# Kernel optimization log

Measured on AMD Instinct MI355X. Metric: run time of the kernel, lower is better.

## Reference

```python
import jax, jax.numpy as jnp
import numpy as np

B, T, D, H = 2, 2048, 1024, 16  # batch, seq, hidden, heads; head_dim = 64


def setup_inputs() -> dict:
    key = jax.random.key(0)
    k1, k2, k3 = jax.random.split(key, 3)
    X = jax.random.normal(k1, (B, T, D), dtype=jnp.float32)
    # Dense(3*hidden_dim, use_bias=False): kernel [D, 3D]
    Wqkv = jax.random.normal(k2, (D, 3 * D), dtype=jnp.float32) / np.float32(np.sqrt(D))
    # Dense(hidden_dim, use_bias=False): kernel [D, D]
    Wproj = jax.random.normal(k3, (D, D), dtype=jnp.float32) / np.float32(np.sqrt(D))
    return {"X": X, "Wqkv": Wqkv, "Wproj": Wproj, "train": 0}


def reference(X, Wqkv, Wproj, train):
    # train=0 -> dropout is identity; the chunked online-softmax in the
    # original is mathematically exact softmax causal attention.
    b, t, d = X.shape
    hd = d // H
    qkv = X @ Wqkv                      # [B,T,3D]
    q, k, v = jnp.split(qkv, 3, axis=-1)
    q = q.reshape(b, t, H, hd)
    k = k.reshape(b, t, H, hd)
    v = v.reshape(b, t, H, hd)
    scale = 1.0 / jnp.sqrt(jnp.asarray(hd, dtype=X.dtype))
    scores = jnp.einsum('bqhd,bkhd->bhqk', q * scale, k)  # [B,H,T,T]
    causal = jnp.tril(jnp.ones((t, t), dtype=bool))
    scores = jnp.where(causal[None, None, :, :], scores, -jnp.inf)
    attn = jax.nn.softmax(scores, axis=-1)
    out = jnp.einsum('bhqk,bkhd->bqhd', attn, v).reshape(b, t, d)
    return out @ Wproj
```

## Files before the change

### kernel.cpp

```cpp
#include <hip/hip_runtime.h>


using u16 = unsigned short;
using u32 = unsigned int;

typedef __bf16 bf16x8 __attribute__((ext_vector_type(8)));
typedef __bf16 bf16x2 __attribute__((ext_vector_type(2)));
typedef float f32x4 __attribute__((ext_vector_type(4)));

#define DEV __device__ __forceinline__

DEV u16 f2bf(float f) { __bf16 h = (__bf16)f; return *(u16*)&h; }

DEV u32 pk2(float lo, float hi) {
  bf16x2 t = {(__bf16)lo, (__bf16)hi};
  return *(u32*)&t;
}

DEV f32x4 mfma16(bf16x8 a, bf16x8 b, f32x4 c) {
  return __builtin_amdgcn_mfma_f32_16x16x32_bf16(a, b, c, 0, 0, 0);
}

DEV void gload_lds16(const void* g, void* l) {
  __builtin_amdgcn_global_load_lds(
      (const __attribute__((address_space(1))) void*)g,
      (__attribute__((address_space(3))) void*)l, 16, 0, 0);
}

DEV bf16x8 ld16(const u16* p) { return *(const bf16x8*)p; }

DEV void BAR() {
  __builtin_amdgcn_s_barrier();
  __builtin_amdgcn_sched_barrier(0);
}

DEV int vperm(int slot) {
  return ((((slot >> 4) & 2) | ((slot >> 2) & 1)) << 4) + (((slot >> 3) & 3) << 2) + (slot & 3);
}


__global__ __launch_bounds__(256) void cvt_x_kernel(const float* __restrict__ X,
                                                    u16* __restrict__ Xb) {
  int i = (blockIdx.x * 256 + threadIdx.x) * 8;
  float4 a = *(const float4*)&X[i];
  float4 b = *(const float4*)&X[i + 4];
  union { u16 u[8]; uint4 v; } o;
  o.u[0] = f2bf(a.x); o.u[1] = f2bf(a.y); o.u[2] = f2bf(a.z); o.u[3] = f2bf(a.w);
  o.u[4] = f2bf(b.x); o.u[5] = f2bf(b.y); o.u[6] = f2bf(b.z); o.u[7] = f2bf(b.w);
  *(uint4*)&Xb[i] = o.v;
}

__global__ __launch_bounds__(256) void transpose_w_kernel(const float* __restrict__ W,
                                                          u16* __restrict__ Wt,
                                                          int R, int C) {
  __shared__ float tile[64][65];
  int tilesC = C >> 6;
  int tr = blockIdx.x / tilesC, tc = blockIdx.x % tilesC;
  int t = threadIdx.x;
#pragma unroll
  for (int j = 0; j < 16; ++j) {
    int idx = j * 256 + t;
    int r = idx >> 6, c = idx & 63;
    tile[r][c] = W[(tr * 64 + r) * C + tc * 64 + c];
  }
  __syncthreads();
#pragma unroll
  for (int j = 0; j < 16; ++j) {
    int idx = j * 256 + t;
    int r = idx >> 6, c = idx & 63;
    Wt[(tc * 64 + r) * R + tr * 64 + c] = f2bf(tile[c][r]);
  }
}

__global__ __launch_bounds__(256) void transpose_v_kernel(const u16* __restrict__ V,
                                                          u16* __restrict__ Vt) {
  __shared__ u16 tile[64 * 65];
  int head = blockIdx.x >> 5, tt = blockIdx.x & 31;
  const u16* src = V + ((size_t)head * 2048 + tt * 64) * 64;
  u16* dst = Vt + (size_t)head * 64 * 2048 + tt * 64;
  int t = threadIdx.x;
#pragma unroll
  for (int it = 0; it < 2; ++it) {
    int idx = it * 2048 + t * 8;
    int r = idx >> 6, c = idx & 63;
    union { uint4 v; u16 u[8]; } tmp;
    tmp.v = *(const uint4*)&src[idx];
#pragma unroll
    for (int j = 0; j < 8; ++j) tile[r * 65 + c + j] = tmp.u[j];
  }
  __syncthreads();
#pragma unroll
  for (int it = 0; it < 2; ++it) {
    int idx = it * 2048 + t * 8;
    int d = idx >> 6, s0 = idx & 63;
    union { uint4 v; u16 u[8]; } tmp;
#pragma unroll
    for (int j = 0; j < 8; ++j) tmp.u[j] = tile[vperm(s0 + j) * 65 + d];
    *(uint4*)&dst[(size_t)d * 2048 + s0] = tmp.v;
  }
}


__global__ __launch_bounds__(512, 2) void gemm256_qkv_kernel(
    const u16* __restrict__ A, const u16* __restrict__ Bt,
    u16* __restrict__ Qb, u16* __restrict__ Kb, u16* __restrict__ Vb) {
  int bid = blockIdx.x;
  int bid2 = (bid & 7) * 24 + (bid >> 3);
  const int mt = bid2 / 12, nt = bid2 % 12;
  const int m0 = mt * 256, n0 = nt * 256;
  const int tid = threadIdx.x;
  const int wid = tid >> 6, lane = tid & 63;
  const int g = lane >> 4, li = lane & 15;
  const int wm = wid >> 2, wn = wid & 3;

  __shared__ __align__(16) u16 lds[65536];

  const int srow = lane >> 3;
  const int scol = ((lane & 7) * 8) ^ ((srow & 7) << 3);

  auto ISSUE = [&](int s, int kt) {
    const int p = kt & 1;
    const u16* base = (s < 2) ? &A[(size_t)(m0 + s * 128) * 1024]
                              : &Bt[(size_t)(n0 + (s - 2) * 128) * 1024];
#pragma unroll
    for (int is2 = 0; is2 < 2; ++is2) {
      int row = is2 * 64 + wid * 8 + srow;
      gload_lds16(&base[(size_t)row * 1024 + kt * 64 + scol],
                  &lds[s * 16384 + p * 8192 + is2 * 4096 + wid * 512]);
    }
  };

  auto LDA = [&](int p, int ks, bf16x8* aF) {
#pragma unroll
    for (int mi = 0; mi < 8; ++mi) {
      int row = mi * 16 + li;
      aF[mi] = ld16(&lds[wm * 16384 + p * 8192 + row * 64 +
                         ((ks * 32 + g * 8) ^ ((li & 7) << 3))]);
    }
  };
  auto LDB = [&](int p, int ks, bf16x8* bF) {
    int s = 2 + (wn >> 1);
#pragma unroll
    for (int ni = 0; ni < 4; ++ni) {
      int row = (wn & 1) * 64 + ni * 16 + li;
      bF[ni] = ld16(&lds[s * 16384 + p * 8192 + row * 64 +
                         ((ks * 32 + g * 8) ^ ((li & 7) << 3))]);
    }
  };

  f32x4 acc[8][4] = {};
  bf16x8 a0[8], a1[8], bF[4];

  ISSUE(0, 0); ISSUE(1, 0); ISSUE(2, 0); ISSUE(3, 0);
  ISSUE(0, 1); ISSUE(1, 1); ISSUE(2, 1);
  asm volatile("s_waitcnt vmcnt(6)" ::: "memory");
  BAR();

  for (int t = 0; t < 16; ++t) {
    const int p = t & 1;
    LDB(p, 0, bF);
    LDA(p, 0, a0);
    if (t + 1 < 16) ISSUE(3, t + 1);
    BAR();
    __builtin_amdgcn_s_setprio(1);
#pragma unroll
    for (int mi = 0; mi < 8; ++mi) {
      acc[mi][0] = mfma16(a0[mi], bF[0], acc[mi][0]);
      acc[mi][1] = mfma16(a0[mi], bF[1], acc[mi][1]);
    }
    __builtin_amdgcn_s_setprio(0);
    BAR();
    LDA(p, 1, a1);
    BAR();
    __builtin_amdgcn_s_setprio(1);
#pragma unroll
    for (int mi = 0; mi < 8; ++mi) {
      acc[mi][2] = mfma16(a0[mi], bF[2], acc[mi][2]);
      acc[mi][3] = mfma16(a0[mi], bF[3], acc[mi][3]);
    }
    __builtin_amdgcn_s_setprio(0);
    BAR();
    LDB(p, 1, bF);
    BAR();
    __builtin_amdgcn_s_setprio(1);
#pragma unroll
    for (int mi = 0; mi < 8; ++mi) {
      acc[mi][0] = mfma16(a1[mi], bF[0], acc[mi][0]);
      acc[mi][1] = mfma16(a1[mi], bF[1], acc[mi][1]);
    }
    __builtin_amdgcn_s_setprio(0);
    BAR();
    if (t + 2 < 16) { ISSUE(0, t + 2); ISSUE(1, t + 2); ISSUE(2, t + 2); }
    BAR();
    __builtin_amdgcn_s_setprio(1);
#pragma unroll
    for (int mi = 0; mi < 8; ++mi) {
      acc[mi][2] = mfma16(a1[mi], bF[2], acc[mi][2]);
      acc[mi][3] = mfma16(a1[mi], bF[3], acc[mi][3]);
    }
    __builtin_amdgcn_s_setprio(0);
    if (t + 2 < 16) {
      asm volatile("s_waitcnt vmcnt(6)" ::: "memory");
    } else {
      asm volatile("s_waitcnt vmcnt(0)" ::: "memory");
    }
    BAR();
  }

#pragma unroll
  for (int mi = 0; mi < 8; ++mi)
#pragma unroll
    for (int ni = 0; ni < 4; ++ni)
#pragma unroll
      for (int r = 0; r < 4; ++r) {
        int rr = m0 + wm * 128 + mi * 16 + g * 4 + r;
        int cc = n0 + wn * 64 + ni * 16 + li;
        float v = acc[mi][ni][r];
        int which = cc >> 10, rem = cc & 1023;
        int h = rem >> 6, dd = rem & 63;
        int bb = rr >> 11, tt = rr & 2047;
        size_t di = ((size_t)(bb * 16 + h) * 2048 + tt) * 64 + dd;
        u16 o = f2bf(which == 0 ? v * 0.18033688f : v);
        (which == 0 ? Qb : which == 1 ? Kb : Vb)[di] = o;
      }
}

__global__ __launch_bounds__(256) void gemm_proj_kernel(
    const u16* __restrict__ A, const u16* __restrict__ Bt, float* __restrict__ OF) {
  constexpr int NTN = 1024 / 128;
  const int mt = blockIdx.x / NTN, nt = blockIdx.x % NTN;
  const int m0 = mt * 128, n0 = nt * 128;
  const int tid = threadIdx.x;
  const int wid = tid >> 6, lane = tid & 63;
  const int g = lane >> 4, li = lane & 15;
  const int wm = wid >> 1, wn = wid & 1;

  __shared__ __align__(16) u16 As[128 * 64];
  __shared__ __align__(16) u16 Bs[128 * 64];

  f32x4 acc[4][4] = {};

  for (int kt = 0; kt < 1024 / 64; ++kt) {
    __syncthreads();
#pragma unroll
    for (int iss = 0; iss < 4; ++iss) {
      int e = iss * 2048 + wid * 512 + lane * 8;
      int row = e >> 6, kk = e & 63;
      gload_lds16(&A[(size_t)(m0 + row) * 1024 + kt * 64 + kk], &As[iss * 2048 + wid * 512]);
      gload_lds16(&Bt[(size_t)(n0 + row) * 1024 + kt * 64 + kk], &Bs[iss * 2048 + wid * 512]);
    }
    __syncthreads();
#pragma unroll
    for (int ks = 0; ks < 2; ++ks) {
      bf16x8 af[4], bfr[4];
#pragma unroll
      for (int mi = 0; mi < 4; ++mi)
        af[mi] = ld16(&As[(wm * 64 + mi * 16 + li) * 64 + ks * 32 + g * 8]);
#pragma unroll
      for (int ni = 0; ni < 4; ++ni)
        bfr[ni] = ld16(&Bs[(wn * 64 + ni * 16 + li) * 64 + ks * 32 + g * 8]);
#pragma unroll
      for (int mi = 0; mi < 4; ++mi)
#pragma unroll
        for (int ni = 0; ni < 4; ++ni)
          acc[mi][ni] = mfma16(af[mi], bfr[ni], acc[mi][ni]);
    }
  }

#pragma unroll
  for (int mi = 0; mi < 4; ++mi)
#pragma unroll
    for (int ni = 0; ni < 4; ++ni)
#pragma unroll
      for (int r = 0; r < 4; ++r) {
        int rr = m0 + wm * 64 + mi * 16 + g * 4 + r;
        int cc = n0 + wn * 64 + ni * 16 + li;
        OF[(size_t)rr * 1024 + cc] = acc[mi][ni][r];
      }
}

__global__ __launch_bounds__(256) void attn_kernel(const u16* __restrict__ Q,
                                                   const u16* __restrict__ K,
                                                   const u16* __restrict__ VtP,
                                                   u16* __restrict__ AO) {
  const int bid = blockIdx.x;
  const int qt = 31 - (bid >> 5);
  const int bh = bid & 31;
  const int b = bh >> 4, h = bh & 15;
  const int tid = threadIdx.x;
  const int wid = tid >> 6, lane = tid & 63;
  const int g = lane >> 4, li = lane & 15;
  const int q0 = qt * 64;

  __shared__ __align__(16) u16 Ks[2][64 * 64];
  __shared__ __align__(16) u16 Vs[2][64 * 64];

  const u16* Qh = Q + (size_t)bh * 2048 * 64;
  const u16* Kh = K + (size_t)bh * 2048 * 64;
  const u16* Vh = VtP + (size_t)bh * 64 * 2048;

  const int qrow = q0 + wid * 16 + li;
  bf16x8 qf[2];
#pragma unroll
  for (int ks = 0; ks < 2; ++ks)
    qf[ks] = ld16(&Qh[(size_t)qrow * 64 + ks * 32 + g * 8]);

  f32x4 accO[4] = {};
  float mrun = -1e30f, lrun = 0.f;

  auto STAGE = [&](int buf, int ktile) {
#pragma unroll
    for (int iss = 0; iss < 2; ++iss) {
      int e = iss * 2048 + wid * 512 + lane * 8;
      int row = e >> 6;
      int c0 = (e & 63) ^ ((row & 7) << 3);
      gload_lds16(&Kh[(size_t)(ktile * 64 + row) * 64 + c0],
                  &Ks[buf][iss * 2048 + wid * 512]);
      gload_lds16(&Vh[(size_t)row * 2048 + ktile * 64 + c0],
                  &Vs[buf][iss * 2048 + wid * 512]);
    }
  };

  STAGE(0, 0);
  int cur = 0;

  for (int kt = 0; kt <= qt; ++kt) {
    __syncthreads();
    if (kt < qt) STAGE(cur ^ 1, kt + 1);

    f32x4 s[4];
#pragma unroll
    for (int ni = 0; ni < 4; ++ni) s[ni] = f32x4{0.f, 0.f, 0.f, 0.f};
#pragma unroll
    for (int ks = 0; ks < 2; ++ks) {
      bf16x8 kf[4];
#pragma unroll
      for (int ni = 0; ni < 4; ++ni)
        kf[ni] = ld16(&Ks[cur][(ni * 16 + li) * 64 + ((ks * 32 + g * 8) ^ ((li & 7) << 3))]);
#pragma unroll
      for (int ni = 0; ni < 4; ++ni) s[ni] = mfma16(kf[ni], qf[ks], s[ni]);
    }

    if (kt == qt) {
      int ql = wid * 16 + li;
#pragma unroll
      for (int ni = 0; ni < 4; ++ni)
#pragma unroll
        for (int r = 0; r < 4; ++r)
          if (ni * 16 + g * 4 + r > ql) s[ni][r] = -1e30f;
    }

    float pmax;
    {
      float m01 = fmaxf(fmaxf(fmaxf(s[0][0], s[0][1]), fmaxf(s[0][2], s[0][3])),
                        fmaxf(fmaxf(s[1][0], s[1][1]), fmaxf(s[1][2], s[1][3])));
      float m23 = fmaxf(fmaxf(fmaxf(s[2][0], s[2][1]), fmaxf(s[2][2], s[2][3])),
                        fmaxf(fmaxf(s[3][0], s[3][1]), fmaxf(s[3][2], s[3][3])));
      pmax = fmaxf(m01, m23);
      pmax = fmaxf(pmax, __shfl_xor(pmax, 16));
      pmax = fmaxf(pmax, __shfl_xor(pmax, 32));
    }

    if (!__all(pmax - mrun <= 8.0f)) {
      float mnew = fmaxf(mrun, pmax);
      float al = exp2f(mrun - mnew);
      mrun = mnew;
      lrun *= al;
#pragma unroll
      for (int mi = 0; mi < 4; ++mi) accO[mi] *= al;
    }

    float rs;
    {
#pragma unroll
      for (int ni = 0; ni < 4; ++ni)
#pragma unroll
        for (int r = 0; r < 4; ++r) s[ni][r] = exp2f(s[ni][r] - mrun);
      float a0 = (s[0][0] + s[0][1]) + (s[0][2] + s[0][3]);
      float a1 = (s[1][0] + s[1][1]) + (s[1][2] + s[1][3]);
      float a2 = (s[2][0] + s[2][1]) + (s[2][2] + s[2][3]);
      float a3 = (s[3][0] + s[3][1]) + (s[3][2] + s[3][3]);
      rs = (a0 + a1) + (a2 + a3);
      rs += __shfl_xor(rs, 16);
      rs += __shfl_xor(rs, 32);
      lrun += rs;
    }

    union { u32 u[4]; bf16x8 v; } pf0, pf1;
    pf0.u[0] = pk2(s[0][0], s[0][1]); pf0.u[1] = pk2(s[0][2], s[0][3]);
    pf0.u[2] = pk2(s[1][0], s[1][1]); pf0.u[3] = pk2(s[1][2], s[1][3]);
    pf1.u[0] = pk2(s[2][0], s[2][1]); pf1.u[1] = pk2(s[2][2], s[2][3]);
    pf1.u[2] = pk2(s[3][0], s[3][1]); pf1.u[3] = pk2(s[3][2], s[3][3]);

#pragma unroll
    for (int ks = 0; ks < 2; ++ks) {
      bf16x8 pf = ks ? pf1.v : pf0.v;
#pragma unroll
      for (int mi = 0; mi < 4; ++mi) {
        bf16x8 vf = ld16(&Vs[cur][(mi * 16 + li) * 64 + ((ks * 32 + g * 8) ^ ((li & 7) << 3))]);
        accO[mi] = mfma16(vf, pf, accO[mi]);
      }
    }
    cur ^= 1;
  }

  float inv = __builtin_amdgcn_rcpf(lrun);
  __syncthreads();
  u16* E = (u16*)Ks;
  int erow = wid * 16 + li;
#pragma unroll
  for (int mi = 0; mi < 4; ++mi) {
    uint2 wv;
    wv.x = pk2(accO[mi][0] * inv, accO[mi][1] * inv);
    wv.y = pk2(accO[mi][2] * inv, accO[mi][3] * inv);
    *(uint2*)&E[erow * 64 + ((mi * 16 + g * 4) ^ ((li & 7) << 3))] = wv;
  }
  __syncthreads();
#pragma unroll
  for (int pass = 0; pass < 2; ++pass) {
    int idx = pass * 2048 + tid * 8;
    int row = idx >> 6, col = idx & 63;
    uint4 val = *(uint4*)&E[row * 64 + (col ^ ((row & 7) << 3))];
    *(uint4*)&AO[(size_t)(b * 2048 + q0 + row) * 1024 + h * 64 + col] = val;
  }
}


extern "C" void kernel_launch(void* const* d_in, const int* in_sizes, int n_in,
                              void* d_out, int out_size, void* d_ws, size_t ws_size,
                              hipStream_t stream) {
  const float* X = (const float*)d_in[0];
  const float* Wqkv = (const float*)d_in[1];
  const float* Wproj = (const float*)d_in[2];
  float* out = (float*)d_out;

  u16* ws = (u16*)d_ws;
  u16* Xb = ws;
  u16* Wqkvt = Xb + 4194304;
  u16* Wprojt = Wqkvt + 3145728;
  u16* Qb = Wprojt + 1048576;
  u16* Kb = Qb + 4194304;
  u16* Vb = Kb + 4194304;
  u16* AO = Vb + 4194304;
  u16* VtP = Xb;

  cvt_x_kernel<<<2048, 256, 0, stream>>>(X, Xb);
  transpose_w_kernel<<<16 * 48, 256, 0, stream>>>(Wqkv, Wqkvt, 1024, 3072);
  transpose_w_kernel<<<16 * 16, 256, 0, stream>>>(Wproj, Wprojt, 1024, 1024);
  gemm256_qkv_kernel<<<192, 512, 0, stream>>>(Xb, Wqkvt, Qb, Kb, Vb);
  transpose_v_kernel<<<1024, 256, 0, stream>>>(Vb, VtP);
  attn_kernel<<<1024, 256, 0, stream>>>(Qb, Kb, VtP, AO);
  gemm_proj_kernel<<<32 * 8, 256, 0, stream>>>(AO, Wprojt, out);
}
```

Baseline: 123.2 us.

## Fuse V transpose into QKV GEMM epilogue and load attention tiles directly from global

The QKV GEMM epilogue now writes V directly in the permuted transposed layout the attention kernel expects, so the separate transpose_v kernel launch and its extra pass over V are removed. The attention kernel also drops LDS double-buffered staging of K and V and instead has each wave load its K and V fragments straight from global memory into registers. This removes barriers and LDS traffic, but every wave now fetches the full K/V tile on its own, with no software prefetch, so load latency is exposed and global traffic rises.

Result: slower. 221.2 us (+79.6%).

```diff
diff --git a/kernel.cpp b/kernel.cpp
--- a/kernel.cpp
+++ b/kernel.cpp
@@ -36,6 +36,9 @@
 
 DEV int vperm(int slot) {
   return ((((slot >> 4) & 2) | ((slot >> 2) & 1)) << 4) + (((slot >> 3) & 3) << 2) + (slot & 3);
+}
+DEV int vperm_inv(int k) {
+  return (k & 0x23) | ((k & 0x10) >> 2) | ((k & 0x0c) << 1);
 }
 
 
@@ -72,38 +75,10 @@
   }
 }
 
-__global__ __launch_bounds__(256) void transpose_v_kernel(const u16* __restrict__ V,
-                                                          u16* __restrict__ Vt) {
-  __shared__ u16 tile[64 * 65];
-  int head = blockIdx.x >> 5, tt = blockIdx.x & 31;
-  const u16* src = V + ((size_t)head * 2048 + tt * 64) * 64;
-  u16* dst = Vt + (size_t)head * 64 * 2048 + tt * 64;
-  int t = threadIdx.x;
-#pragma unroll
-  for (int it = 0; it < 2; ++it) {
-    int idx = it * 2048 + t * 8;
-    int r = idx >> 6, c = idx & 63;
-    union { uint4 v; u16 u[8]; } tmp;
-    tmp.v = *(const uint4*)&src[idx];
-#pragma unroll
-    for (int j = 0; j < 8; ++j) tile[r * 65 + c + j] = tmp.u[j];
-  }
-  __syncthreads();
-#pragma unroll
-  for (int it = 0; it < 2; ++it) {
-    int idx = it * 2048 + t * 8;
-    int d = idx >> 6, s0 = idx & 63;
-    union { uint4 v; u16 u[8]; } tmp;
-#pragma unroll
-    for (int j = 0; j < 8; ++j) tmp.u[j] = tile[vperm(s0 + j) * 65 + d];
-    *(uint4*)&dst[(size_t)d * 2048 + s0] = tmp.v;
-  }
-}
-
 
 __global__ __launch_bounds__(512, 2) void gemm256_qkv_kernel(
     const u16* __restrict__ A, const u16* __restrict__ Bt,
-    u16* __restrict__ Qb, u16* __restrict__ Kb, u16* __restrict__ Vb) {
+    u16* __restrict__ Qb, u16* __restrict__ Kb, u16* __restrict__ VtP) {
   int bid = blockIdx.x;
   int bid2 = (bid & 7) * 24 + (bid >> 3);
   const int mt = bid2 / 12, nt = bid2 % 12;
@@ -210,19 +185,27 @@
 #pragma unroll
   for (int mi = 0; mi < 8; ++mi)
 #pragma unroll
-    for (int ni = 0; ni < 4; ++ni)
-#pragma unroll
-      for (int r = 0; r < 4; ++r) {
-        int rr = m0 + wm * 128 + mi * 16 + g * 4 + r;
-        int cc = n0 + wn * 64 + ni * 16 + li;
-        float v = acc[mi][ni][r];
-        int which = cc >> 10, rem = cc & 1023;
-        int h = rem >> 6, dd = rem & 63;
-        int bb = rr >> 11, tt = rr & 2047;
+    for (int ni = 0; ni < 4; ++ni) {
+      int cc = n0 + wn * 64 + ni * 16 + li;
+      int which = cc >> 10, rem = cc & 1023;
+      int h = rem >> 6, dd = rem & 63;
+      int rbase = m0 + wm * 128 + mi * 16 + g * 4;
+      int bb = rbase >> 11, tt = rbase & 2047;
+      if (which == 2) {
+        int slot0 = (tt & ~63) + vperm_inv(tt & 63);
+        size_t di = ((size_t)(bb * 16 + h) * 64 + dd) * 2048 + slot0;
+        uint2 wv;
+        wv.x = pk2(acc[mi][ni][0], acc[mi][ni][1]);
+        wv.y = pk2(acc[mi][ni][2], acc[mi][ni][3]);
+        *(uint2*)&VtP[di] = wv;
+      } else {
+        u16* dst = which == 0 ? Qb : Kb;
+        float sc = which == 0 ? 0.18033688f : 1.0f;
         size_t di = ((size_t)(bb * 16 + h) * 2048 + tt) * 64 + dd;
-        u16 o = f2bf(which == 0 ? v * 0.18033688f : v);
-        (which == 0 ? Qb : which == 1 ? Kb : Vb)[di] = o;
+#pragma unroll
+        for (int r = 0; r < 4; ++r) dst[di + (size_t)r * 64] = f2bf(acc[mi][ni][r] * sc);
       }
+    }
 }
 
 __global__ __launch_bounds__(256) void gemm_proj_kernel(
@@ -278,6 +261,7 @@
         OF[(size_t)rr * 1024 + cc] = acc[mi][ni][r];
       }
 }
+
 
 __global__ __launch_bounds__(256) void attn_kernel(const u16* __restrict__ Q,
                                                    const u16* __restrict__ K,
@@ -292,8 +276,7 @@
   const int g = lane >> 4, li = lane & 15;
   const int q0 = qt * 64;
 
-  __shared__ __align__(16) u16 Ks[2][64 * 64];
-  __shared__ __align__(16) u16 Vs[2][64 * 64];
+  __shared__ __align__(16) u16 E[64 * 64];
 
   const u16* Qh = Q + (size_t)bh * 2048 * 64;
   const u16* Kh = K + (size_t)bh * 2048 * 64;
@@ -308,38 +291,27 @@
   f32x4 accO[4] = {};
   float mrun = -1e30f, lrun = 0.f;
 
-  auto STAGE = [&](int buf, int ktile) {
-#pragma unroll
-    for (int iss = 0; iss < 2; ++iss) {
-      int e = iss * 2048 + wid * 512 + lane * 8;
-      int row = e >> 6;
-      int c0 = (e & 63) ^ ((row & 7) << 3);
-      gload_lds16(&Kh[(size_t)(ktile * 64 + row) * 64 + c0],
-                  &Ks[buf][iss * 2048 + wid * 512]);
-      gload_lds16(&Vh[(size_t)row * 2048 + ktile * 64 + c0],
-                  &Vs[buf][iss * 2048 + wid * 512]);
-    }
-  };
-
-  STAGE(0, 0);
-  int cur = 0;
-
   for (int kt = 0; kt <= qt; ++kt) {
-    __syncthreads();
-    if (kt < qt) STAGE(cur ^ 1, kt + 1);
+    const u16* Kt = &Kh[(size_t)kt * 64 * 64];
+    bf16x8 kf[8], vf[8];
+#pragma unroll
+    for (int ni = 0; ni < 4; ++ni) {
+      kf[ni]     = ld16(&Kt[(ni * 16 + li) * 64 + g * 8]);
+      kf[4 + ni] = ld16(&Kt[(ni * 16 + li) * 64 + 32 + g * 8]);
+    }
+#pragma unroll
+    for (int mi = 0; mi < 4; ++mi) {
+      vf[mi]     = ld16(&Vh[(size_t)(mi * 16 + li) * 2048 + kt * 64 + g * 8]);
+      vf[4 + mi] = ld16(&Vh[(size_t)(mi * 16 + li) * 2048 + kt * 64 + 32 + g * 8]);
+    }
 
     f32x4 s[4];
 #pragma unroll
     for (int ni = 0; ni < 4; ++ni) s[ni] = f32x4{0.f, 0.f, 0.f, 0.f};
 #pragma unroll
-    for (int ks = 0; ks < 2; ++ks) {
-      bf16x8 kf[4];
-#pragma unroll
-      for (int ni = 0; ni < 4; ++ni)
-        kf[ni] = ld16(&Ks[cur][(ni * 16 + li) * 64 + ((ks * 32 + g * 8) ^ ((li & 7) << 3))]);
-#pragma unroll
-      for (int ni = 0; ni < 4; ++ni) s[ni] = mfma16(kf[ni], qf[ks], s[ni]);
-    }
+    for (int ni = 0; ni < 4; ++ni) s[ni] = mfma16(kf[ni], qf[0], s[ni]);
+#pragma unroll
+    for (int ni = 0; ni < 4; ++ni) s[ni] = mfma16(kf[4 + ni], qf[1], s[ni]);
 
     if (kt == qt) {
       int ql = wid * 16 + li;
@@ -393,20 +365,12 @@
     pf1.u[2] = pk2(s[3][0], s[3][1]); pf1.u[3] = pk2(s[3][2], s[3][3]);
 
 #pragma unroll
-    for (int ks = 0; ks < 2; ++ks) {
-      bf16x8 pf = ks ? pf1.v : pf0.v;
-#pragma unroll
-      for (int mi = 0; mi < 4; ++mi) {
-        bf16x8 vf = ld16(&Vs[cur][(mi * 16 + li) * 64 + ((ks * 32 + g * 8) ^ ((li & 7) << 3))]);
-        accO[mi] = mfma16(vf, pf, accO[mi]);
-      }
-    }
-    cur ^= 1;
+    for (int mi = 0; mi < 4; ++mi) accO[mi] = mfma16(vf[mi], pf0.v, accO[mi]);
+#pragma unroll
+    for (int mi = 0; mi < 4; ++mi) accO[mi] = mfma16(vf[4 + mi], pf1.v, accO[mi]);
   }
 
   float inv = __builtin_amdgcn_rcpf(lrun);
-  __syncthreads();
-  u16* E = (u16*)Ks;
   int erow = wid * 16 + li;
 #pragma unroll
   for (int mi = 0; mi < 4; ++mi) {
@@ -440,15 +404,13 @@
   u16* Wprojt = Wqkvt + 3145728;
   u16* Qb = Wprojt + 1048576;
   u16* Kb = Qb + 4194304;
-  u16* Vb = Kb + 4194304;
-  u16* AO = Vb + 4194304;
-  u16* VtP = Xb;
+  u16* VtP = Kb + 4194304;
+  u16* AO = VtP + 4194304;
 
   cvt_x_kernel<<<2048, 256, 0, stream>>>(X, Xb);
   transpose_w_kernel<<<16 * 48, 256, 0, stream>>>(Wqkv, Wqkvt, 1024, 3072);
   transpose_w_kernel<<<16 * 16, 256, 0, stream>>>(Wproj, Wprojt, 1024, 1024);
-  gemm256_qkv_kernel<<<192, 512, 0, stream>>>(Xb, Wqkvt, Qb, Kb, Vb);
-  transpose_v_kernel<<<1024, 256, 0, stream>>>(Vb, VtP);
+  gemm256_qkv_kernel<<<192, 512, 0, stream>>>(Xb, Wqkvt, Qb, Kb, VtP);
   attn_kernel<<<1024, 256, 0, stream>>>(Qb, Kb, VtP, AO);
   gemm_proj_kernel<<<32 * 8, 256, 0, stream>>>(AO, Wprojt, out);
 }
```
